# Optimization experiments

Measured on AMD Instinct MI355X. Metric: run time of the kernel, lower is better.

Reference implementation:

```python
import jax, jax.numpy as jnp
import numpy as np

TOP_K = 2
NEG_INF = -1.0e9


def setup_inputs() -> dict:
    key = jax.random.key(0)
    k = jax.random.split(key, 5)
    B, S, D, E = 4, 2048, 1024, 8
    H = 2 * D
    x = jax.random.normal(k[0], (B, S, D), dtype=jnp.float32)
    gate_w = jax.random.normal(k[1], (D, E), dtype=jnp.float32) * 0.02
    gate_b = jnp.zeros((E,), dtype=jnp.float32)
    w1 = jax.random.normal(k[2], (E, D, H), dtype=jnp.float32) * 0.02
    b1 = jnp.zeros((E, H), dtype=jnp.float32)
    w2 = jax.random.normal(k[3], (E, H, D), dtype=jnp.float32) * 0.02
    b2 = jnp.zeros((E, D), dtype=jnp.float32)
    noise = jax.random.normal(k[4], (B, S, E), dtype=jnp.float32)
    return {"x": x, "gate_w": gate_w, "gate_b": gate_b,
            "w1": w1, "b1": b1, "w2": w2, "b2": b2, "noise": noise}


def reference(x, gate_w, gate_b, w1, b1, w2, b2, noise):
    B, S, D = x.shape
    # Gating: linear + small gaussian noise (hk.next_rng_key equivalent)
    gating_logits = jnp.einsum('bsd,de->bse', x, gate_w) + gate_b + noise * 0.01
    # keep_top_k: mask all but top-k logits to -1e9
    top_k_values, top_k_indices = jax.lax.top_k(gating_logits, TOP_K)
    mask = gating_logits >= jnp.min(top_k_values, axis=-1, keepdims=True)
    gating_logits = jnp.where(mask, gating_logits, NEG_INF)
    gating_probs = jax.nn.softmax(gating_logits, axis=-1)
    # Dense compute of ALL experts on ALL tokens (as in source): [E,B,S,D]
    h = jax.nn.silu(jnp.einsum('bsd,edh->ebsh', x, w1) + b1[:, None, None, :])
    expert_outputs = jnp.einsum('ebsh,ehd->ebsd', h, w2) + b2[:, None, None, :]
    # Gather top-k expert outputs per token: [B,S,K,D]
    bi = jnp.arange(B)[:, None, None]
    si = jnp.arange(S)[None, :, None]
    selected = expert_outputs[top_k_indices, bi, si]
    top_k_gating_probs = jnp.take_along_axis(gating_probs, top_k_indices, axis=-1)
    final_output = jnp.einsum('bskd,bsk->bsd', selected, top_k_gating_probs)
    # Load-balancing aux loss on the MASKED logits (as in source)
    routing_probs = jax.nn.softmax(gating_logits, axis=-1)
    expert_usage = jnp.sum(routing_probs, axis=(0, 1))
    expert_importance = expert_usage / jnp.sum(expert_usage)
    mean_imp = jnp.mean(expert_importance)
    std_imp = jnp.std(expert_importance)
    aux_loss = std_imp / (mean_imp + 1e-10)
    return final_output, top_k_indices, aux_loss
```

## Files before the change

### kernel.cpp

```cpp
#include <hip/hip_runtime.h>
#include <stdint.h>


#define NTOK   8192
#define DIM    1024
#define NEXP   8
#define HID    2048
#define OUT_MAIN (NTOK * DIM)
#define IDX_OFF  OUT_MAIN
#define AUX_OFF  (OUT_MAIN + NTOK * 2)
#define MAXBLK 72

typedef __attribute__((ext_vector_type(8))) short short8;
typedef __attribute__((ext_vector_type(4))) float floatx4;

__device__ __forceinline__ unsigned short f2bf(float f) {
  unsigned int b = __float_as_uint(f);
  b += 0x7FFFu + ((b >> 16) & 1u);
  return (unsigned short)(b >> 16);
}

__global__ __launch_bounds__(1024) void k_gating(
    const float* __restrict__ x, const float* __restrict__ gate_w,
    const float* __restrict__ gate_b, const float* __restrict__ noise,
    float* __restrict__ out, int* __restrict__ counts,
    int* __restrict__ lists_tok, float* __restrict__ lists_p,
    float* __restrict__ probs_all, unsigned short* __restrict__ xb)
{
  const int lane = threadIdx.x & 63;
  const int wv   = threadIdx.x >> 6;
  const int t    = blockIdx.x * 16 + wv;
  const float* xr = x + (size_t)t * DIM;

  __shared__ int   cnt[NEXP];
  __shared__ int   base[NEXP];
  __shared__ int   s_e[32];
  __shared__ int   s_pos[32];
  __shared__ float s_p[32];
  if (threadIdx.x < NEXP) cnt[threadIdx.x] = 0;

  double acc[NEXP] = {0,0,0,0,0,0,0,0};
  #pragma unroll
  for (int jj = 0; jj < 4; ++jj) {
    const int d0 = lane * 4 + jj * 256;
    const float4 xv = *(const float4*)(xr + d0);
    const float xs[4] = {xv.x, xv.y, xv.z, xv.w};
    unsigned short xbq[4];
    #pragma unroll
    for (int c = 0; c < 4; ++c) {
      const float4 g0 = *(const float4*)(gate_w + (size_t)(d0 + c) * NEXP);
      const float4 g1 = *(const float4*)(gate_w + (size_t)(d0 + c) * NEXP + 4);
      const double xd = (double)xs[c];
      acc[0] += xd * (double)g0.x; acc[1] += xd * (double)g0.y;
      acc[2] += xd * (double)g0.z; acc[3] += xd * (double)g0.w;
      acc[4] += xd * (double)g1.x; acc[5] += xd * (double)g1.y;
      acc[6] += xd * (double)g1.z; acc[7] += xd * (double)g1.w;
      xbq[c] = f2bf(xs[c]);
    }
    ushort4 q; q.x = xbq[0]; q.y = xbq[1]; q.z = xbq[2]; q.w = xbq[3];
    *(ushort4*)(xb + (size_t)t * DIM + d0) = q;
  }
  #pragma unroll
  for (int e = 0; e < NEXP; ++e) {
    #pragma unroll
    for (int off = 32; off; off >>= 1) acc[e] += __shfl_xor(acc[e], off);
  }
  __syncthreads();
  if (lane == 0) {
    double l[NEXP];
    #pragma unroll
    for (int e = 0; e < NEXP; ++e)
      l[e] = acc[e] + (double)gate_b[e] + 0.01 * (double)noise[(size_t)t * NEXP + e];
    int i1 = 0; double v1 = l[0];
    #pragma unroll
    for (int e = 1; e < NEXP; ++e) if (l[e] > v1) { v1 = l[e]; i1 = e; }
    int i2 = (i1 == 0) ? 1 : 0; double v2 = l[i2];
    #pragma unroll
    for (int e = 0; e < NEXP; ++e) if (e != i1 && l[e] > v2) { v2 = l[e]; i2 = e; }
    float pr[NEXP]; float Z = 0.f;
    #pragma unroll
    for (int e = 0; e < NEXP; ++e) {
      const float a = (l[e] >= v2) ? (float)(l[e] - v1) : -1.0e9f;
      pr[e] = __expf(a); Z += pr[e];
    }
    const float rz = 1.0f / Z;
    #pragma unroll
    for (int e = 0; e < NEXP; ++e) {
      pr[e] *= rz;
      probs_all[(size_t)t * NEXP + e] = pr[e];
    }
    out[(size_t)IDX_OFF + t * 2]     = (float)i1;
    out[(size_t)IDX_OFF + t * 2 + 1] = (float)i2;
    const int p1 = atomicAdd(&cnt[i1], 1);
    const int p2 = atomicAdd(&cnt[i2], 1);
    s_e[wv * 2]     = i1; s_pos[wv * 2]     = p1; s_p[wv * 2]     = pr[i1];
    s_e[wv * 2 + 1] = i2; s_pos[wv * 2 + 1] = p2; s_p[wv * 2 + 1] = pr[i2];
  }
  __syncthreads();
  if (threadIdx.x < NEXP) base[threadIdx.x] = atomicAdd(&counts[threadIdx.x], cnt[threadIdx.x]);
  __syncthreads();
  if (lane == 0) {
    #pragma unroll
    for (int k = 0; k < 2; ++k) {
      const int ee  = s_e[wv * 2 + k];
      const int pos = base[ee] + s_pos[wv * 2 + k];
      lists_tok[ee * NTOK + pos] = t;
      lists_p[ee * NTOK + pos]   = s_p[wv * 2 + k];
    }
  }
}

__global__ void k_offs(const int* __restrict__ counts, int* __restrict__ offs,
                       int* __restrict__ tbl_e, int* __restrict__ tbl_m,
                       int* __restrict__ nblk) {
  if (threadIdx.x == 0) {
    int a = 0;
    #pragma unroll
    for (int e = 0; e < NEXP; ++e) { offs[e] = a; a += counts[e]; }
    offs[NEXP] = a;
    int nb = 0;
    for (int e = 0; e < NEXP; ++e) {
      const int nbe = (counts[e] + 255) >> 8;
      for (int m = 0; m < nbe; ++m) { tbl_e[nb] = e; tbl_m[nb] = m << 8; ++nb; }
    }
    nblk[0] = nb;
    for (int b = nb; b < MAXBLK; ++b) { tbl_e[b] = 0; tbl_m[b] = 0; }
  }
}

__global__ __launch_bounds__(256) void k_aux(const float* __restrict__ probs_all,
                                             float* __restrict__ out) {
  float p[NEXP] = {0,0,0,0,0,0,0,0};
  for (int t = threadIdx.x; t < NTOK; t += 256) {
    const float4 a = *(const float4*)(probs_all + (size_t)t * NEXP);
    const float4 b = *(const float4*)(probs_all + (size_t)t * NEXP + 4);
    p[0] += a.x; p[1] += a.y; p[2] += a.z; p[3] += a.w;
    p[4] += b.x; p[5] += b.y; p[6] += b.z; p[7] += b.w;
  }
  #pragma unroll
  for (int e = 0; e < NEXP; ++e) {
    #pragma unroll
    for (int off = 32; off; off >>= 1) p[e] += __shfl_xor(p[e], off);
  }
  __shared__ float red[4][NEXP];
  const int lane = threadIdx.x & 63, wv = threadIdx.x >> 6;
  if (lane == 0) {
    #pragma unroll
    for (int e = 0; e < NEXP; ++e) red[wv][e] = p[e];
  }
  __syncthreads();
  if (threadIdx.x == 0) {
    float usage[NEXP], s = 0.f;
    #pragma unroll
    for (int e = 0; e < NEXP; ++e) {
      usage[e] = red[0][e] + red[1][e] + red[2][e] + red[3][e];
      s += usage[e];
    }
    float imp[NEXP], mean = 0.f, var = 0.f;
    #pragma unroll
    for (int e = 0; e < NEXP; ++e) { imp[e] = usage[e] / s; mean += imp[e]; }
    mean *= 0.125f;
    #pragma unroll
    for (int e = 0; e < NEXP; ++e) { const float d = imp[e] - mean; var += d * d; }
    var *= 0.125f;
    out[AUX_OFF] = sqrtf(var) / (mean + 1e-10f);
  }
}

__global__ __launch_bounds__(256) void k_tr(
    const float* __restrict__ in, unsigned short* __restrict__ out,
    int in_ld, size_t in_estride, int r0, int c0,
    int out_ld, size_t out_estride)
{
  const int e  = blockIdx.z;
  const int tr = blockIdx.x << 6;
  const int tc = blockIdx.y << 6;
  const int tid = threadIdx.x;
  __shared__ float t[64][65];
  const float* src = in + (size_t)e * in_estride + (size_t)(r0 + tr) * in_ld + (c0 + tc);
  #pragma unroll
  for (int p = 0; p < 4; ++p) {
    const int r  = (p << 4) + (tid >> 4);
    const int c4 = (tid & 15) << 2;
    const float4 v = *(const float4*)(src + (size_t)r * in_ld + c4);
    t[r][c4] = v.x; t[r][c4 + 1] = v.y; t[r][c4 + 2] = v.z; t[r][c4 + 3] = v.w;
  }
  __syncthreads();
  unsigned short* dst = out + (size_t)e * out_estride + (size_t)tc * out_ld + tr;
  #pragma unroll
  for (int p = 0; p < 4; ++p) {
    const int c  = (p << 4) + (tid >> 4);
    const int r4 = (tid & 15) << 2;
    ushort4 q;
    q.x = f2bf(t[r4][c]);     q.y = f2bf(t[r4 + 1][c]);
    q.z = f2bf(t[r4 + 2][c]); q.w = f2bf(t[r4 + 3][c]);
    *(ushort4*)(dst + (size_t)c * out_ld + r4) = q;
  }
}

template <int MODE>
__global__ __launch_bounds__(1024) void k_gemm(
    const unsigned short* __restrict__ Abase,
    const unsigned short* __restrict__ Bt,
    const float* __restrict__ bias,
    const int* __restrict__ counts, const int* __restrict__ offs,
    const int* __restrict__ tbl_e, const int* __restrict__ tbl_m,
    const int* __restrict__ nblk,
    const int* __restrict__ lists_tok, const float* __restrict__ lists_p,
    unsigned short* __restrict__ hout, float* __restrict__ out,
    const int hb, const int Hs)
{
  const int lin = blockIdx.y * gridDim.x + blockIdx.x;
  const int qc  = gridDim.x >> 3;
  const int jl  = lin >> 3;
  const int bx  = (lin & 7) * qc + jl / gridDim.y;
  const int by  = jl % gridDim.y;
  if (bx >= nblk[0]) return;
  const int e   = tbl_e[bx];
  const int m0  = tbl_m[bx];
  const int n_e = counts[e];

  int nb, k0g, Kloc;
  if (MODE == 0) { nb = by << 8; k0g = 0; Kloc = DIM; }
  else { nb = (by >> 1) << 8; const int half = Hs >> 1;
         k0g = (by & 1) * half; Kloc = half; }

  const int tid  = threadIdx.x;
  const int lane = tid & 63;
  const int wv   = tid >> 6;
  const int wm   = (wv & 3) << 6;
  const int wn   = (wv >> 2) << 6;

  __shared__ __align__(16) unsigned short as[2][256 * 32];
  __shared__ __align__(16) unsigned short bs[2][256 * 32];

  const int K = (MODE == 0) ? DIM : Hs;
  const unsigned short* Bexp = Bt + (size_t)e * ((size_t)DIM * Hs) + (size_t)nb * K + k0g;

  const int swk   = (((lane & 3) ^ ((lane >> 2) & 3)) << 3);
  const int rbase = wv << 4;
  const int r     = rbase + (lane >> 2);
  const int rcA   = (m0 + r < n_e) ? (m0 + r) : (n_e - 1);
  size_t arow;
  if (MODE == 0) arow = (size_t)lists_tok[e * NTOK + rcA] * DIM;
  else           arow = (size_t)(offs[e] + rcA) * Hs;
  const unsigned short* gpa = Abase + arow + k0g + swk;
  const unsigned short* gpb = Bexp + (size_t)r * K + swk;
  unsigned short* lpa0 = &as[0][rbase << 5];
  unsigned short* lpb0 = &bs[0][rbase << 5];
  unsigned short* lpa1 = &as[1][rbase << 5];
  unsigned short* lpb1 = &bs[1][rbase << 5];

  floatx4 acc[4][4];
  #pragma unroll
  for (int i = 0; i < 4; ++i)
    #pragma unroll
    for (int j2 = 0; j2 < 4; ++j2) acc[i][j2] = (floatx4){0.f, 0.f, 0.f, 0.f};

  auto issue = [&](int buf, int kko) {
    __builtin_amdgcn_global_load_lds(
        (const __attribute__((address_space(1))) void*)(gpa + kko),
        (__attribute__((address_space(3))) void*)(void*)(buf ? lpa1 : lpa0), 16, 0, 0);
    __builtin_amdgcn_global_load_lds(
        (const __attribute__((address_space(1))) void*)(gpb + kko),
        (__attribute__((address_space(3))) void*)(void*)(buf ? lpb1 : lpb0), 16, 0, 0);
  };

  issue(0, 0);
  int p = 0;
  for (int kk = 0; kk < Kloc; kk += 32) {
    __syncthreads();
    if (kk + 32 < Kloc) issue(p ^ 1, kk + 32);
    const int c = lane >> 4;
    short8 af[4];
    #pragma unroll
    for (int i = 0; i < 4; ++i) {
      const int row = wm + (i << 4) + (lane & 15);
      af[i] = *(const short8*)(&as[p][(row << 5) + ((c ^ (row & 3)) << 3)]);
    }
    short8 bfr[4];
    #pragma unroll
    for (int j2 = 0; j2 < 4; ++j2) {
      const int row = wn + (j2 << 4) + (lane & 15);
      bfr[j2] = *(const short8*)(&bs[p][(row << 5) + ((c ^ (row & 3)) << 3)]);
    }
    #pragma unroll
    for (int i = 0; i < 4; ++i)
      #pragma unroll
      for (int j2 = 0; j2 < 4; ++j2)
        acc[i][j2] = __builtin_amdgcn_mfma_f32_16x16x32_bf16(af[i], bfr[j2], acc[i][j2], 0, 0, 0);
    p ^= 1;
  }

  const int q4 = (lane >> 4) << 2;
  if (MODE == 0) {
    #pragma unroll
    for (int i = 0; i < 4; ++i) {
      #pragma unroll
      for (int j2 = 0; j2 < 4; ++j2) {
        const int nloc = wn + (j2 << 4) + (lane & 15);
        const float bb = bias[e * HID + hb + nb + nloc];
        #pragma unroll
        for (int rr = 0; rr < 4; ++rr) {
          const int m = m0 + wm + (i << 4) + q4 + rr;
          if (m < n_e) {
            float v = acc[i][j2][rr] + bb;
            v = v / (1.0f + __expf(-v));
            hout[(size_t)(offs[e] + m) * Hs + nb + nloc] = f2bf(v);
          }
        }
      }
    }
  } else {
    #pragma unroll
    for (int i = 0; i < 4; ++i) {
      #pragma unroll
      for (int rr = 0; rr < 4; ++rr) {
        const int m = m0 + wm + (i << 4) + q4 + rr;
        if (m < n_e) {
          const int   tok = lists_tok[e * NTOK + m];
          const float pp  = lists_p[e * NTOK + m];
          #pragma unroll
          for (int j2 = 0; j2 < 4; ++j2) {
            const int d = nb + wn + (j2 << 4) + (lane & 15);
            float v = acc[i][j2][rr];
            if (hb == 0 && k0g == 0) v += bias[e * DIM + d];
            atomicAdd(out + (size_t)tok * DIM + d, pp * v);
          }
        }
      }
    }
  }
}

extern "C" void kernel_launch(void* const* d_in, const int* in_sizes, int n_in,
                              void* d_out, int out_size, void* d_ws, size_t ws_size,
                              hipStream_t stream)
{
  const float* x      = (const float*)d_in[0];
  const float* gate_w = (const float*)d_in[1];
  const float* gate_b = (const float*)d_in[2];
  const float* w1     = (const float*)d_in[3];
  const float* b1     = (const float*)d_in[4];
  const float* w2     = (const float*)d_in[5];
  const float* b2     = (const float*)d_in[6];
  const float* noise  = (const float*)d_in[7];
  float* out = (float*)d_out;

  char* ws = (char*)d_ws;
  const size_t CNT_OFF = 0;
  const size_t OFF_OFF = 64;
  const size_t NBK_OFF = 128;
  const size_t TBE_OFF = 192;
  const size_t TBM_OFF = 1024;
  const size_t LT_OFF  = 2048;
  const size_t LP_OFF  = LT_OFF + 262144;
  const size_t PA_OFF  = LP_OFF + 262144;
  const size_t XB_OFF  = 1048576;
  const size_t W_OFF   = 17825792;

  int nsl = 0;
  for (int cand = 1; cand <= 8; cand <<= 1) {
    const size_t need = W_OFF + (size_t)(33554432 + 67108864) / (size_t)cand;
    if (ws_size >= need) { nsl = cand; break; }
  }
  if (!nsl) return;
  const int Hs = HID / nsl;

  int* counts          = (int*)(ws + CNT_OFF);
  int* offs            = (int*)(ws + OFF_OFF);
  int* nblk            = (int*)(ws + NBK_OFF);
  int* tbl_e           = (int*)(ws + TBE_OFF);
  int* tbl_m           = (int*)(ws + TBM_OFF);
  int* lists_tok       = (int*)(ws + LT_OFF);
  float* lists_p       = (float*)(ws + LP_OFF);
  float* probs_all     = (float*)(ws + PA_OFF);
  unsigned short* xb   = (unsigned short*)(ws + XB_OFF);
  unsigned short* wt   = (unsigned short*)(ws + W_OFF);
  unsigned short* hbuf = (unsigned short*)(ws + W_OFF + (size_t)33554432 / nsl);

  hipMemsetAsync(d_out, 0, (size_t)OUT_MAIN * sizeof(float), stream);
  hipMemsetAsync(ws + CNT_OFF, 0, 64, stream);

  k_gating<<<NTOK / 16, 1024, 0, stream>>>(x, gate_w, gate_b, noise, out, counts,
                                           lists_tok, lists_p, probs_all, xb);
  k_offs<<<1, 64, 0, stream>>>(counts, offs, tbl_e, tbl_m, nblk);
  k_aux<<<1, 256, 0, stream>>>(probs_all, out);

  for (int s = 0; s < nsl; ++s) {
    const int hb = s * Hs;
    dim3 gt1(DIM / 64, Hs / 64, NEXP);
    k_tr<<<gt1, 256, 0, stream>>>(w1, wt, HID, (size_t)DIM * HID, 0, hb,
                                  DIM, (size_t)Hs * DIM);
    dim3 g1(MAXBLK, Hs / 256, 1);
    k_gemm<0><<<g1, 1024, 0, stream>>>(xb, wt, b1, counts, offs, tbl_e, tbl_m, nblk,
                                       lists_tok, lists_p, hbuf, out, hb, Hs);
    dim3 gt2(Hs / 64, DIM / 64, NEXP);
    k_tr<<<gt2, 256, 0, stream>>>(w2, wt, DIM, (size_t)DIM * HID, hb, 0,
                                  Hs, (size_t)DIM * Hs);
    dim3 g2(MAXBLK, (DIM / 256) * 2, 1);
    k_gemm<1><<<g2, 1024, 0, stream>>>(hbuf, wt, b2, counts, offs, tbl_e, tbl_m, nblk,
                                       lists_tok, lists_p, hbuf, out, hb, Hs);
  }
}
```

Measured before the change: 438.4 us.

## Deepen GEMM K-tile to 64 with prefetch-two pipeline and swizzled block table

Doubles the K tile per shared-memory stage from 32 to 64, preloads two stages and uses explicit vmcnt waits with raw barriers so global-to-LDS loads overlap MFMA work, and raises wave priority around the MFMA bursts. It also moves the XCD-aware block remapping from the GEMM kernel into the offsets kernel, which writes a pre-interleaved table with -1 sentinels, so blocks index it directly. LDS use doubles, which may lower occupancy, and the hand-placed waitcnt logic is fragile.

```diff
diff --git a/kernel.cpp b/kernel.cpp
--- a/kernel.cpp
+++ b/kernel.cpp
@@ -118,13 +118,24 @@
     #pragma unroll
     for (int e = 0; e < NEXP; ++e) { offs[e] = a; a += counts[e]; }
     offs[NEXP] = a;
+    int ent_e[MAXBLK], ent_m[MAXBLK];
     int nb = 0;
     for (int e = 0; e < NEXP; ++e) {
       const int nbe = (counts[e] + 255) >> 8;
-      for (int m = 0; m < nbe; ++m) { tbl_e[nb] = e; tbl_m[nb] = m << 8; ++nb; }
+      for (int m = 0; m < nbe; ++m) { ent_e[nb] = e; ent_m[nb] = m << 8; ++nb; }
     }
     nblk[0] = nb;
-    for (int b = nb; b < MAXBLK; ++b) { tbl_e[b] = 0; tbl_m[b] = 0; }
+    for (int p = 0; p < MAXBLK; ++p) { tbl_e[p] = -1; tbl_m[p] = 0; }
+    const int q = nb >> 3, r = nb & 7;
+    for (int c = 0; c < 8; ++c) {
+      const int cnt   = q + (c < r ? 1 : 0);
+      const int start = c * q + (c < r ? c : r);
+      for (int t = 0; t < cnt; ++t) {
+        const int pos = c + (t << 3);
+        tbl_e[pos] = ent_e[start + t];
+        tbl_m[pos] = ent_m[start + t];
+      }
+    }
   }
 }
 
@@ -210,15 +221,12 @@
     unsigned short* __restrict__ hout, float* __restrict__ out,
     const int hb, const int Hs)
 {
-  const int lin = blockIdx.y * gridDim.x + blockIdx.x;
-  const int qc  = gridDim.x >> 3;
-  const int jl  = lin >> 3;
-  const int bx  = (lin & 7) * qc + jl / gridDim.y;
-  const int by  = jl % gridDim.y;
-  if (bx >= nblk[0]) return;
-  const int e   = tbl_e[bx];
+  const int bx = blockIdx.x;
+  const int e  = tbl_e[bx];
+  if (e < 0) return;
   const int m0  = tbl_m[bx];
   const int n_e = counts[e];
+  const int by  = blockIdx.y;
 
   int nb, k0g, Kloc;
   if (MODE == 0) { nb = by << 8; k0g = 0; Kloc = DIM; }
@@ -231,25 +239,29 @@
   const int wm   = (wv & 3) << 6;
   const int wn   = (wv >> 2) << 6;
 
-  __shared__ __align__(16) unsigned short as[2][256 * 32];
-  __shared__ __align__(16) unsigned short bs[2][256 * 32];
+  __shared__ __align__(16) unsigned short as[2][256 * 64];
+  __shared__ __align__(16) unsigned short bs[2][256 * 64];
 
   const int K = (MODE == 0) ? DIM : Hs;
   const unsigned short* Bexp = Bt + (size_t)e * ((size_t)DIM * Hs) + (size_t)nb * K + k0g;
 
-  const int swk   = (((lane & 3) ^ ((lane >> 2) & 3)) << 3);
-  const int rbase = wv << 4;
-  const int r     = rbase + (lane >> 2);
-  const int rcA   = (m0 + r < n_e) ? (m0 + r) : (n_e - 1);
-  size_t arow;
-  if (MODE == 0) arow = (size_t)lists_tok[e * NTOK + rcA] * DIM;
-  else           arow = (size_t)(offs[e] + rcA) * Hs;
-  const unsigned short* gpa = Abase + arow + k0g + swk;
-  const unsigned short* gpb = Bexp + (size_t)r * K + swk;
-  unsigned short* lpa0 = &as[0][rbase << 5];
-  unsigned short* lpb0 = &bs[0][rbase << 5];
-  unsigned short* lpa1 = &as[1][rbase << 5];
-  unsigned short* lpb1 = &bs[1][rbase << 5];
+  const int off_sh = ((lane & 7) ^ (lane >> 3)) << 3;
+  const int Ra0 = wv * 8 + (lane >> 3);
+  const int Ra1 = 128 + Ra0;
+  const int rc0 = (m0 + Ra0 < n_e) ? (m0 + Ra0) : (n_e - 1);
+  const int rc1 = (m0 + Ra1 < n_e) ? (m0 + Ra1) : (n_e - 1);
+  size_t arow0, arow1;
+  if (MODE == 0) {
+    arow0 = (size_t)lists_tok[e * NTOK + rc0] * DIM;
+    arow1 = (size_t)lists_tok[e * NTOK + rc1] * DIM;
+  } else {
+    arow0 = (size_t)(offs[e] + rc0) * Hs;
+    arow1 = (size_t)(offs[e] + rc1) * Hs;
+  }
+  const unsigned short* gpa0 = Abase + arow0 + k0g + off_sh;
+  const unsigned short* gpa1 = Abase + arow1 + k0g + off_sh;
+  const unsigned short* gpb0 = Bexp + (size_t)Ra0 * K + off_sh;
+  const unsigned short* gpb1 = Bexp + (size_t)Ra1 * K + off_sh;
 
   floatx4 acc[4][4];
   #pragma unroll
@@ -257,38 +269,61 @@
     #pragma unroll
     for (int j2 = 0; j2 < 4; ++j2) acc[i][j2] = (floatx4){0.f, 0.f, 0.f, 0.f};
 
-  auto issue = [&](int buf, int kko) {
+  auto issue = [&](int buf, int kk) {
+    unsigned short* a0 = (buf ? &as[1][0] : &as[0][0]) + wv * 8 * 64;
+    unsigned short* b0 = (buf ? &bs[1][0] : &bs[0][0]) + wv * 8 * 64;
     __builtin_amdgcn_global_load_lds(
-        (const __attribute__((address_space(1))) void*)(gpa + kko),
-        (__attribute__((address_space(3))) void*)(void*)(buf ? lpa1 : lpa0), 16, 0, 0);
+        (const __attribute__((address_space(1))) void*)(gpa0 + kk),
+        (__attribute__((address_space(3))) void*)(void*)a0, 16, 0, 0);
     __builtin_amdgcn_global_load_lds(
-        (const __attribute__((address_space(1))) void*)(gpb + kko),
-        (__attribute__((address_space(3))) void*)(void*)(buf ? lpb1 : lpb0), 16, 0, 0);
+        (const __attribute__((address_space(1))) void*)(gpa1 + kk),
+        (__attribute__((address_space(3))) void*)(void*)(a0 + 128 * 64), 16, 0, 0);
+    __builtin_amdgcn_global_load_lds(
+        (const __attribute__((address_space(1))) void*)(gpb0 + kk),
+        (__attribute__((address_space(3))) void*)(void*)b0, 16, 0, 0);
+    __builtin_amdgcn_global_load_lds(
+        (const __attribute__((address_space(1))) void*)(gpb1 + kk),
+        (__attribute__((address_space(3))) void*)(void*)(b0 + 128 * 64), 16, 0, 0);
   };
 
+  const int nt = Kloc >> 6;
   issue(0, 0);
+  issue(1, 64);
   int p = 0;
-  for (int kk = 0; kk < Kloc; kk += 32) {
-    __syncthreads();
-    if (kk + 32 < Kloc) issue(p ^ 1, kk + 32);
+  for (int t = 0; t < nt; ++t) {
+    if (t + 1 < nt) { asm volatile("s_waitcnt vmcnt(4)" ::: "memory"); }
+    else            { asm volatile("s_waitcnt vmcnt(0)" ::: "memory"); }
+    __builtin_amdgcn_sched_barrier(0);
+    __builtin_amdgcn_s_barrier();
+    __builtin_amdgcn_sched_barrier(0);
+    const unsigned short* ap = p ? &as[1][0] : &as[0][0];
+    const unsigned short* bp = p ? &bs[1][0] : &bs[0][0];
     const int c = lane >> 4;
-    short8 af[4];
-    #pragma unroll
-    for (int i = 0; i < 4; ++i) {
-      const int row = wm + (i << 4) + (lane & 15);
-      af[i] = *(const short8*)(&as[p][(row << 5) + ((c ^ (row & 3)) << 3)]);
-    }
-    short8 bfr[4];
-    #pragma unroll
-    for (int j2 = 0; j2 < 4; ++j2) {
-      const int row = wn + (j2 << 4) + (lane & 15);
-      bfr[j2] = *(const short8*)(&bs[p][(row << 5) + ((c ^ (row & 3)) << 3)]);
-    }
-    #pragma unroll
-    for (int i = 0; i < 4; ++i)
+    #pragma unroll
+    for (int s = 0; s < 2; ++s) {
+      short8 af[4], bfr[4];
       #pragma unroll
-      for (int j2 = 0; j2 < 4; ++j2)
-        acc[i][j2] = __builtin_amdgcn_mfma_f32_16x16x32_bf16(af[i], bfr[j2], acc[i][j2], 0, 0, 0);
+      for (int i = 0; i < 4; ++i) {
+        const int row = wm + (i << 4) + (lane & 15);
+        af[i] = *(const short8*)(ap + row * 64 + ((((s << 2) | c) ^ (row & 7)) << 3));
+      }
+      #pragma unroll
+      for (int j2 = 0; j2 < 4; ++j2) {
+        const int row = wn + (j2 << 4) + (lane & 15);
+        bfr[j2] = *(const short8*)(bp + row * 64 + ((((s << 2) | c) ^ (row & 7)) << 3));
+      }
+      __builtin_amdgcn_s_setprio(1);
+      #pragma unroll
+      for (int i = 0; i < 4; ++i)
+        #pragma unroll
+        for (int j2 = 0; j2 < 4; ++j2)
+          acc[i][j2] = __builtin_amdgcn_mfma_f32_16x16x32_bf16(af[i], bfr[j2], acc[i][j2], 0, 0, 0);
+      __builtin_amdgcn_s_setprio(0);
+    }
+    __builtin_amdgcn_sched_barrier(0);
+    __builtin_amdgcn_s_barrier();
+    __builtin_amdgcn_sched_barrier(0);
+    if (t + 2 < nt) issue(p, (t + 2) << 6);
     p ^= 1;
   }
 
```

Measured after the change: 409.0 us. 6.7% less time.
